# Performance work log

Hardware: AMD Instinct MI355X
Metric: run time of the kernel (lower is better)

The kernel has to match this reference:

```python
import jax, jax.numpy as jnp
import numpy as np

V, D, H, L, FF, C = 32000, 512, 8, 3, 2048, 6
B, S = 32, 1024


def setup_inputs() -> dict:
    key = jax.random.key(0)
    ks = jax.random.split(key, 8)
    tokens = jax.random.randint(ks[0], (B, S), 0, V, dtype=jnp.int32)
    emb = jax.random.normal(ks[1], (V, D), dtype=jnp.float32) * 0.02
    qkv_w = jax.random.normal(ks[2], (L, D, 3 * D), dtype=jnp.float32) * (D ** -0.5)
    qkv_b = jnp.zeros((L, 3 * D), dtype=jnp.float32)
    fc_w = jax.random.normal(ks[3], (L, D, D), dtype=jnp.float32) * (D ** -0.5)
    fc_b = jnp.zeros((L, D), dtype=jnp.float32)
    gamma = jnp.ones((D,), dtype=jnp.float32)
    beta = jnp.zeros((D,), dtype=jnp.float32)
    fc1_w = jax.random.normal(ks[4], (D, FF), dtype=jnp.float32) * (D ** -0.5)
    fc1_b = jnp.zeros((FF,), dtype=jnp.float32)
    fc2_w = jax.random.normal(ks[5], (FF, C), dtype=jnp.float32) * (FF ** -0.5)
    fc2_b = jnp.zeros((C,), dtype=jnp.float32)
    return dict(tokens=tokens, emb=emb, qkv_w=qkv_w, qkv_b=qkv_b, fc_w=fc_w,
                fc_b=fc_b, gamma=gamma, beta=beta, fc1_w=fc1_w, fc1_b=fc1_b,
                fc2_w=fc2_w, fc2_b=fc2_b)


def _sinusoidal_pe(seq_len, dim):
    pos = jnp.arange(seq_len, dtype=jnp.float32)[:, None]
    div = jnp.exp(jnp.arange(0, dim, 2).astype(jnp.float32) * (-np.log(10000.0) / dim))
    pe = jnp.zeros((seq_len, dim), dtype=jnp.float32)
    pe = pe.at[:, 0::2].set(jnp.sin(pos * div))
    pe = pe.at[:, 1::2].set(jnp.cos(pos * div))
    return pe


def reference(tokens, emb, qkv_w, qkv_b, fc_w, fc_b, gamma, beta, fc1_w, fc1_b, fc2_w, fc2_b):
    b, s = tokens.shape
    dh = D // H
    scale = dh ** -0.5

    def layernorm(y):
        m = y.mean(-1, keepdims=True)
        v = ((y - m) ** 2).mean(-1, keepdims=True)
        return (y - m) * jax.lax.rsqrt(v + 1e-5) * gamma + beta

    x = emb[tokens] + _sinusoidal_pe(s, D)[None]  # [B,S,D]
    for l in range(L):
        qkv = (x @ qkv_w[l] + qkv_b[l]).reshape(b, s, H, 3, dh)
        q = qkv[..., 0, :].transpose(0, 2, 1, 3)  # [B,H,S,dh]
        k = qkv[..., 1, :].transpose(0, 2, 1, 3)
        v = qkv[..., 2, :].transpose(0, 2, 1, 3)
        attn = jax.nn.softmax(jnp.einsum('bhqd,bhkd->bhqk', q, k) * scale, axis=-1)
        o = jnp.einsum('bhqk,bhkd->bhqd', attn, v).transpose(0, 2, 1, 3).reshape(b, s, D)
        o = o @ fc_w[l] + fc_b[l]
        x = layernorm(o + x)
    pooled = x.mean(axis=1)  # [B,D]
    h = jax.nn.relu(pooled @ fc1_w + fc1_b)  # dropout is identity at inference
    return h @ fc2_w + fc2_b
```

## Files before the change

kernel.cpp:

```cpp
#include <hip/hip_runtime.h>
#include <cmath>

#define BS_TOK 32768
#define DMODEL 512
#define NHEAD 8
#define DHEAD 64
#define NLAYER 3
#define FFDIM 2048
#define NCLS 6
#define BATCH 32
#define SEQ 1024
#define QKVW 1536

typedef short short8 __attribute__((ext_vector_type(8)));
typedef float float4v __attribute__((ext_vector_type(4)));
#define MFMA_BF16 __builtin_amdgcn_mfma_f32_16x16x32_bf16
#define QSCALE 0.18033688011112042f

__device__ __forceinline__ unsigned short f2bf(float x) {
    return (unsigned short)((__float_as_uint(x) + 0x8000u) >> 16);
}

__global__ __launch_bounds__(128) void embed_pe_kernel(const int* __restrict__ tokens,
                                                       const float* __restrict__ emb,
                                                       float* __restrict__ X,
                                                       unsigned short* __restrict__ Xb) {
    int t = blockIdx.x;
    int pos = t & (SEQ - 1);
    int tok = tokens[t];
    int d0 = threadIdx.x * 4;
    float4 e = *(const float4*)(emb + (size_t)tok * DMODEL + d0);
    const float c = -9.210340371976184f / 512.0f;
    float div0 = expf((float)d0 * c);
    float div1 = expf((float)(d0 + 2) * c);
    float a0 = (float)pos * div0;
    float a1 = (float)pos * div1;
    e.x += sinf(a0); e.y += cosf(a0);
    e.z += sinf(a1); e.w += cosf(a1);
    *(float4*)(X + (size_t)t * DMODEL + d0) = e;
    *(ushort4*)(Xb + (size_t)t * DMODEL + d0) =
        make_ushort4(f2bf(e.x), f2bf(e.y), f2bf(e.z), f2bf(e.w));
}

__global__ __launch_bounds__(256) void transcvt_kernel(const float* __restrict__ in,
                                                       unsigned short* __restrict__ out,
                                                       int R, int C) {
    __shared__ float t[32][33];
    size_t base = (size_t)blockIdx.z * R * C;
    int c0 = blockIdx.x * 32, r0 = blockIdx.y * 32;
    int tx = threadIdx.x & 31, ty = threadIdx.x >> 5;
#pragma unroll
    for (int i = 0; i < 4; i++)
        t[ty + i * 8][tx] = in[base + (size_t)(r0 + ty + i * 8) * C + c0 + tx];
    __syncthreads();
#pragma unroll
    for (int i = 0; i < 4; i++)
        out[base + (size_t)(c0 + ty + i * 8) * R + r0 + tx] = f2bf(t[tx][ty + i * 8]);
}

__global__ __launch_bounds__(256) void transcvt_qkv_kernel(const float* __restrict__ in,
                                                           unsigned short* __restrict__ out) {
    __shared__ float t[32][33];
    int l = blockIdx.z;
    int n0 = blockIdx.x * 32, r0 = blockIdx.y * 32;
    int seg = n0 >> 9, nn = n0 & 511, h = nn >> 6, d0 = nn & 63;
    int c0 = h * 192 + seg * 64 + d0;
    float s = (seg == 0) ? QSCALE : 1.f;
    const float* inp = in + (size_t)l * DMODEL * QKVW;
    unsigned short* op = out + (size_t)l * QKVW * DMODEL;
    int tx = threadIdx.x & 31, ty = threadIdx.x >> 5;
#pragma unroll
    for (int i = 0; i < 4; i++)
        t[ty + i * 8][tx] = inp[(size_t)(r0 + ty + i * 8) * QKVW + c0 + tx];
    __syncthreads();
#pragma unroll
    for (int i = 0; i < 4; i++)
        op[(size_t)(n0 + ty + i * 8) * DMODEL + r0 + tx] = f2bf(t[tx][ty + i * 8] * s);
}

__global__ __launch_bounds__(256) void permbias_kernel(const float* __restrict__ qkv_b,
                                                       float* __restrict__ pb) {
    int i = blockIdx.x * 256 + threadIdx.x;
    int l = i / QKVW, n = i - l * QKVW;
    int seg = n >> 9, nn = n & 511, h = nn >> 6, d = nn & 63;
    float s = (seg == 0) ? QSCALE : 1.f;
    pb[i] = qkv_b[l * QKVW + h * 192 + seg * 64 + d] * s;
}

__global__ __launch_bounds__(256) void gemm_qkv_kernel(const unsigned short* __restrict__ A,
                                                       const unsigned short* __restrict__ Bt,
                                                       const float* __restrict__ pb,
                                                       unsigned short* __restrict__ QKc,
                                                       unsigned short* __restrict__ Vt,
                                                       int M) {
    __shared__ unsigned short As[128 * 40];
    __shared__ unsigned short Bs[128 * 40];
    int bm = blockIdx.y * 128, bn = blockIdx.x * 128;
    int tid = threadIdx.x;
    int w = tid >> 6, lane = tid & 63, l15 = lane & 15, quad = lane >> 4;
    int wm = (w & 1) * 64, wn = (w >> 1) * 64;

    float4v acc[4][4];
    float4v z = {0.f, 0.f, 0.f, 0.f};
#pragma unroll
    for (int i = 0; i < 4; i++)
#pragma unroll
        for (int j = 0; j < 4; j++) acc[i][j] = z;

    int r0 = tid >> 2, o0 = (tid & 3) * 8;
    int r1 = (tid + 256) >> 2, o1 = (tid & 3) * 8;

    for (int k0 = 0; k0 < DMODEL; k0 += 32) {
        __syncthreads();
        *(short8*)&As[r0 * 40 + o0] = *(const short8*)(A + (size_t)(bm + r0) * DMODEL + k0 + o0);
        *(short8*)&As[r1 * 40 + o1] = *(const short8*)(A + (size_t)(bm + r1) * DMODEL + k0 + o1);
        *(short8*)&Bs[r0 * 40 + o0] = *(const short8*)(Bt + (size_t)(bn + r0) * DMODEL + k0 + o0);
        *(short8*)&Bs[r1 * 40 + o1] = *(const short8*)(Bt + (size_t)(bn + r1) * DMODEL + k0 + o1);
        __syncthreads();
        short8 af[4], bf[4];
#pragma unroll
        for (int i = 0; i < 4; i++)
            af[i] = *(short8*)&As[(wm + i * 16 + l15) * 40 + quad * 8];
#pragma unroll
        for (int j = 0; j < 4; j++)
            bf[j] = *(short8*)&Bs[(wn + j * 16 + l15) * 40 + quad * 8];
#pragma unroll
        for (int i = 0; i < 4; i++)
#pragma unroll
            for (int j = 0; j < 4; j++)
                acc[i][j] = MFMA_BF16(af[i], bf[j], acc[i][j], 0, 0, 0);
    }

    float bj[4];
#pragma unroll
    for (int j = 0; j < 4; j++) bj[j] = pb[bn + wn + j * 16 + l15];

    if (bn < 1024) {
#pragma unroll
        for (int i = 0; i < 4; i++)
#pragma unroll
            for (int r = 0; r < 4; r++) {
                size_t row = (size_t)(bm + wm + i * 16 + quad * 4 + r);
#pragma unroll
                for (int j = 0; j < 4; j++)
                    QKc[row * 1024 + bn + wn + j * 16 + l15] = f2bf(acc[i][j][r] + bj[j]);
            }
    } else {
        int bl = bm >> 10;
        int sbase = (bm & 1023) + wm;
#pragma unroll
        for (int j = 0; j < 4; j++) {
            int colp = bn - 1024 + wn + j * 16 + l15;
            int h = colp >> 6, d = colp & 63;
            unsigned short* vb = Vt + ((size_t)(bl * 8 + h) * 64 + d) * 1024 + sbase;
#pragma unroll
            for (int i = 0; i < 4; i++) {
                ushort4 v4 = make_ushort4(f2bf(acc[i][j][0] + bj[j]),
                                          f2bf(acc[i][j][1] + bj[j]),
                                          f2bf(acc[i][j][2] + bj[j]),
                                          f2bf(acc[i][j][3] + bj[j]));
                *(ushort4*)(vb + i * 16 + quad * 4) = v4;
            }
        }
    }
}

__global__ __launch_bounds__(256) void attn_kernel(const unsigned short* __restrict__ QKc,
                                                   const unsigned short* __restrict__ Vt,
                                                   unsigned short* __restrict__ O) {
    __shared__ unsigned short Ks[64 * 72];
    __shared__ unsigned short Vts[64 * 72];
    __shared__ unsigned short Ps[4 * 32 * 72];
    int bh = blockIdx.y;
    int b = bh >> 3, h = bh & 7;
    int q0 = blockIdx.x * 128;
    int tid = threadIdx.x;
    int w = tid >> 6, lane = tid & 63, l15 = lane & 15, quad = lane >> 4;
    unsigned short* Psb = &Ps[w * 32 * 72];
    const unsigned short* Kg = QKc + (size_t)b * SEQ * 1024 + 512 + h * 64;
    const unsigned short* Vg = Vt + (size_t)bh * 64 * 1024;

    short8 qf[2][2];
#pragma unroll
    for (int i = 0; i < 2; i++) {
        const unsigned short* qb =
            QKc + (size_t)(b * SEQ + q0 + w * 32 + i * 16 + l15) * 1024 + h * 64;
        qf[i][0] = *(const short8*)(qb + quad * 8);
        qf[i][1] = *(const short8*)(qb + 32 + quad * 8);
    }

    float lsum[2][4] = {{0.f, 0.f, 0.f, 0.f}, {0.f, 0.f, 0.f, 0.f}};
    float4v accO[2][4];
    float4v z = {0.f, 0.f, 0.f, 0.f};
#pragma unroll
    for (int i = 0; i < 2; i++)
#pragma unroll
        for (int dc = 0; dc < 4; dc++) accO[i][dc] = z;

    int sr = tid >> 2, so = (tid & 3) * 16;

    for (int jt = 0; jt < SEQ / 64; jt++) {
        __syncthreads();
        {
            const unsigned short* kg = Kg + (size_t)(jt * 64 + sr) * 1024 + so;
            *(short8*)&Ks[sr * 72 + so] = *(const short8*)kg;
            *(short8*)&Ks[sr * 72 + so + 8] = *(const short8*)(kg + 8);
            const unsigned short* vg = Vg + (size_t)sr * 1024 + jt * 64 + so;
            *(short8*)&Vts[sr * 72 + so] = *(const short8*)vg;
            *(short8*)&Vts[sr * 72 + so + 8] = *(const short8*)(vg + 8);
        }
        __syncthreads();

        float4v sv[2][4];
#pragma unroll
        for (int jc = 0; jc < 4; jc++) {
            short8 kf0 = *(short8*)&Ks[(jc * 16 + l15) * 72 + quad * 8];
            short8 kf1 = *(short8*)&Ks[(jc * 16 + l15) * 72 + 32 + quad * 8];
#pragma unroll
            for (int i = 0; i < 2; i++) {
                float4v s = MFMA_BF16(qf[i][0], kf0, z, 0, 0, 0);
                sv[i][jc] = MFMA_BF16(qf[i][1], kf1, s, 0, 0, 0);
            }
        }

#pragma unroll
        for (int i = 0; i < 2; i++)
#pragma unroll
            for (int jc = 0; jc < 4; jc++)
#pragma unroll
                for (int r = 0; r < 4; r++) {
                    float p = exp2f(sv[i][jc][r]);
                    lsum[i][r] += p;
                    Psb[(i * 16 + quad * 4 + r) * 72 + jc * 16 + l15] = f2bf(p);
                }

        short8 pf[2][2];
#pragma unroll
        for (int i = 0; i < 2; i++) {
            pf[i][0] = *(short8*)&Psb[(i * 16 + l15) * 72 + quad * 8];
            pf[i][1] = *(short8*)&Psb[(i * 16 + l15) * 72 + 32 + quad * 8];
        }

#pragma unroll
        for (int dc = 0; dc < 4; dc++) {
            short8 vf0 = *(short8*)&Vts[(dc * 16 + l15) * 72 + quad * 8];
            short8 vf1 = *(short8*)&Vts[(dc * 16 + l15) * 72 + 32 + quad * 8];
#pragma unroll
            for (int i = 0; i < 2; i++) {
                accO[i][dc] = MFMA_BF16(pf[i][0], vf0, accO[i][dc], 0, 0, 0);
                accO[i][dc] = MFMA_BF16(pf[i][1], vf1, accO[i][dc], 0, 0, 0);
            }
        }
    }

#pragma unroll
    for (int i = 0; i < 2; i++)
#pragma unroll
        for (int r = 0; r < 4; r++) {
            float s = lsum[i][r];
#pragma unroll
            for (int mask = 1; mask < 16; mask <<= 1) s += __shfl_xor(s, mask);
            float rinv = 1.f / s;
            size_t row = (size_t)(b * SEQ + q0 + w * 32 + i * 16 + quad * 4 + r);
#pragma unroll
            for (int dc = 0; dc < 4; dc++)
                O[row * DMODEL + h * DHEAD + dc * 16 + l15] = f2bf(accO[i][dc][r] * rinv);
        }
}

__global__ __launch_bounds__(256) void proj_ln_kernel(const unsigned short* __restrict__ A,
                                                      const unsigned short* __restrict__ Bt,
                                                      const float* __restrict__ bias,
                                                      const float* __restrict__ gamma,
                                                      const float* __restrict__ beta,
                                                      float* __restrict__ X,
                                                      unsigned short* __restrict__ Xb) {
    __shared__ unsigned short As[32 * 40];
    __shared__ unsigned short Bs[512 * 40];
    __shared__ float redS[4][32], redQ[4][32];
    int bm = blockIdx.x * 32;
    int tid = threadIdx.x;
    int w = tid >> 6, lane = tid & 63, l15 = lane & 15, quad = lane >> 4;
    int wn = w * 128;

    float4v acc[2][8];
    float4v z = {0.f, 0.f, 0.f, 0.f};
#pragma unroll
    for (int i = 0; i < 2; i++)
#pragma unroll
        for (int j = 0; j < 8; j++) acc[i][j] = z;

    for (int k0 = 0; k0 < DMODEL; k0 += 32) {
        __syncthreads();
        if (tid < 128) {
            int r = tid >> 2, o = (tid & 3) * 8;
            *(short8*)&As[r * 40 + o] = *(const short8*)(A + (size_t)(bm + r) * DMODEL + k0 + o);
        }
#pragma unroll
        for (int u = 0; u < 8; u++) {
            int c = tid + u * 256;
            int r = c >> 2, o = (c & 3) * 8;
            *(short8*)&Bs[r * 40 + o] = *(const short8*)(Bt + (size_t)r * DMODEL + k0 + o);
        }
        __syncthreads();
        short8 af[2];
#pragma unroll
        for (int i = 0; i < 2; i++)
            af[i] = *(short8*)&As[(i * 16 + l15) * 40 + quad * 8];
#pragma unroll
        for (int j = 0; j < 8; j++) {
            short8 bf = *(short8*)&Bs[(wn + j * 16 + l15) * 40 + quad * 8];
            acc[0][j] = MFMA_BF16(af[0], bf, acc[0][j], 0, 0, 0);
            acc[1][j] = MFMA_BF16(af[1], bf, acc[1][j], 0, 0, 0);
        }
    }

    float bj[8], g[8], be[8];
#pragma unroll
    for (int j = 0; j < 8; j++) {
        int col = wn + j * 16 + l15;
        bj[j] = bias[col]; g[j] = gamma[col]; be[j] = beta[col];
    }

    float o[2][4][8];
#pragma unroll
    for (int i = 0; i < 2; i++)
#pragma unroll
        for (int r = 0; r < 4; r++) {
            int lrow = i * 16 + quad * 4 + r;
            size_t row = (size_t)(bm + lrow);
            float ss = 0.f, qq = 0.f;
#pragma unroll
            for (int j = 0; j < 8; j++) {
                float v = acc[i][j][r] + bj[j] + X[row * DMODEL + wn + j * 16 + l15];
                o[i][r][j] = v; ss += v; qq += v * v;
            }
#pragma unroll
            for (int mask = 1; mask < 16; mask <<= 1) {
                ss += __shfl_xor(ss, mask);
                qq += __shfl_xor(qq, mask);
            }
            if (l15 == 0) { redS[w][lrow] = ss; redQ[w][lrow] = qq; }
        }
    __syncthreads();
#pragma unroll
    for (int i = 0; i < 2; i++)
#pragma unroll
        for (int r = 0; r < 4; r++) {
            int lrow = i * 16 + quad * 4 + r;
            float S = redS[0][lrow] + redS[1][lrow] + redS[2][lrow] + redS[3][lrow];
            float Q = redQ[0][lrow] + redQ[1][lrow] + redQ[2][lrow] + redQ[3][lrow];
            float mean = S * (1.f / 512.f);
            float var = Q * (1.f / 512.f) - mean * mean;
            float rstd = rsqrtf(var + 1e-5f);
            size_t row = (size_t)(bm + lrow);
#pragma unroll
            for (int j = 0; j < 8; j++) {
                float n = (o[i][r][j] - mean) * rstd * g[j] + be[j];
                X[row * DMODEL + wn + j * 16 + l15] = n;
                Xb[row * DMODEL + wn + j * 16 + l15] = f2bf(n);
            }
        }
}

__global__ __launch_bounds__(256) void zero_kernel(float* __restrict__ p) {
    p[blockIdx.x * 256 + threadIdx.x] = 0.f;
}
__global__ __launch_bounds__(128) void pool_kernel(const float* __restrict__ X,
                                                   float* __restrict__ pooled) {
    int b = blockIdx.x, ch = blockIdx.y;
    int d0 = threadIdx.x * 4;
    float4 acc = make_float4(0.f, 0.f, 0.f, 0.f);
    const float* base = X + (size_t)(b * SEQ + ch * 64) * DMODEL + d0;
    for (int s2 = 0; s2 < 64; s2++) {
        float4 v = *(const float4*)(base + (size_t)s2 * DMODEL);
        acc.x += v.x; acc.y += v.y; acc.z += v.z; acc.w += v.w;
    }
    atomicAdd(pooled + b * DMODEL + d0 + 0, acc.x);
    atomicAdd(pooled + b * DMODEL + d0 + 1, acc.y);
    atomicAdd(pooled + b * DMODEL + d0 + 2, acc.z);
    atomicAdd(pooled + b * DMODEL + d0 + 3, acc.w);
}

__global__ __launch_bounds__(256) void fc1_kernel(const float* __restrict__ pooled,
                                                  const float* __restrict__ fc1_w,
                                                  const float* __restrict__ fc1_b,
                                                  float* __restrict__ h) {
    __shared__ float p[DMODEL];
    int ffc = blockIdx.x, b = blockIdx.y;
    int tid = threadIdx.x;
    p[tid] = pooled[b * DMODEL + tid] * (1.f / 1024.f);
    p[tid + 256] = pooled[b * DMODEL + tid + 256] * (1.f / 1024.f);
    __syncthreads();
    int ff = ffc * 256 + tid;
    float acc = fc1_b[ff];
    for (int k = 0; k < DMODEL; k++) acc += p[k] * fc1_w[(size_t)k * FFDIM + ff];
    h[(size_t)b * FFDIM + ff] = fmaxf(acc, 0.f);
}

__global__ __launch_bounds__(256) void fc2_kernel(const float* __restrict__ h,
                                                  const float* __restrict__ fc2_w,
                                                  const float* __restrict__ fc2_b,
                                                  float* __restrict__ out) {
    __shared__ float red[NCLS][256];
    int b = blockIdx.x, tid = threadIdx.x;
    float a[NCLS];
#pragma unroll
    for (int c = 0; c < NCLS; c++) a[c] = 0.f;
    int k0 = tid * 8;
#pragma unroll
    for (int u = 0; u < 8; u++) {
        float hv = h[(size_t)b * FFDIM + k0 + u];
#pragma unroll
        for (int c = 0; c < NCLS; c++) a[c] += hv * fc2_w[(k0 + u) * NCLS + c];
    }
#pragma unroll
    for (int c = 0; c < NCLS; c++) red[c][tid] = a[c];
    __syncthreads();
    if (tid < NCLS) {
        float s = 0.f;
        for (int i = 0; i < 256; i++) s += red[tid][i];
        out[b * NCLS + tid] = s + fc2_b[tid];
    }
}

extern "C" void kernel_launch(void* const* d_in, const int* in_sizes, int n_in,
                              void* d_out, int out_size, void* d_ws, size_t ws_size,
                              hipStream_t stream) {
    const int* tokens = (const int*)d_in[0];
    const float* emb = (const float*)d_in[1];
    const float* qkv_w = (const float*)d_in[2];
    const float* qkv_b = (const float*)d_in[3];
    const float* fc_w = (const float*)d_in[4];
    const float* fc_b = (const float*)d_in[5];
    const float* gamma = (const float*)d_in[6];
    const float* beta = (const float*)d_in[7];
    const float* fc1_w = (const float*)d_in[8];
    const float* fc1_b = (const float*)d_in[9];
    const float* fc2_w = (const float*)d_in[10];
    const float* fc2_b = (const float*)d_in[11];
    float* out = (float*)d_out;

    char* p = (char*)d_ws;
    float* X = (float*)p;                         p += (size_t)BS_TOK * DMODEL * 4;
    unsigned short* Xb = (unsigned short*)p;      p += (size_t)BS_TOK * DMODEL * 2;
    float* pooled = (float*)p;                    p += (size_t)BATCH * DMODEL * 4;
    float* hbuf = (float*)p;                      p += (size_t)BATCH * FFDIM * 4;
    float* pb = (float*)p;                        p += (size_t)NLAYER * QKVW * 4;
    unsigned short* qkv_wbt = (unsigned short*)p; p += (size_t)NLAYER * QKVW * DMODEL * 2;
    unsigned short* fc_wt = (unsigned short*)p;   p += (size_t)NLAYER * DMODEL * DMODEL * 2;
    size_t fixed_bytes = (size_t)(p - (char*)d_ws);
    size_t per_batch = (size_t)SEQ * 1024 * 2 + (size_t)NHEAD * 64 * SEQ * 2
                     + (size_t)SEQ * DMODEL * 2;
    int chunkB = 1;
    for (int cb = 32; cb >= 1; cb >>= 1)
        if (fixed_bytes + (size_t)cb * per_batch <= ws_size) { chunkB = cb; break; }
    unsigned short* QKc = (unsigned short*)p;     p += (size_t)chunkB * SEQ * 1024 * 2;
    unsigned short* Vt = (unsigned short*)p;      p += (size_t)chunkB * NHEAD * 64 * SEQ * 2;
    unsigned short* Oc = (unsigned short*)p;
    int rows = chunkB * SEQ;
    int nchunks = BATCH / chunkB;

    embed_pe_kernel<<<BS_TOK, 128, 0, stream>>>(tokens, emb, X, Xb);
    permbias_kernel<<<NLAYER * QKVW / 256, 256, 0, stream>>>(qkv_b, pb);
    transcvt_qkv_kernel<<<dim3(QKVW / 32, DMODEL / 32, NLAYER), 256, 0, stream>>>(
        qkv_w, qkv_wbt);
    transcvt_kernel<<<dim3(DMODEL / 32, DMODEL / 32, NLAYER), 256, 0, stream>>>(
        fc_w, fc_wt, DMODEL, DMODEL);

    for (int l = 0; l < NLAYER; l++) {
        for (int c = 0; c < nchunks; c++) {
            unsigned short* Xbc = Xb + (size_t)c * rows * DMODEL;
            float* Xc = X + (size_t)c * rows * DMODEL;
            gemm_qkv_kernel<<<dim3(QKVW / 128, rows / 128), 256, 0, stream>>>(
                Xbc, qkv_wbt + (size_t)l * QKVW * DMODEL, pb + (size_t)l * QKVW,
                QKc, Vt, rows);
            attn_kernel<<<dim3(SEQ / 128, chunkB * NHEAD), 256, 0, stream>>>(QKc, Vt, Oc);
            proj_ln_kernel<<<rows / 32, 256, 0, stream>>>(
                Oc, fc_wt + (size_t)l * DMODEL * DMODEL, fc_b + (size_t)l * DMODEL,
                gamma, beta, Xc, Xbc);
        }
    }

    zero_kernel<<<BATCH * DMODEL / 256, 256, 0, stream>>>(pooled);
    pool_kernel<<<dim3(BATCH, 16), 128, 0, stream>>>(X, pooled);
    fc1_kernel<<<dim3(FFDIM / 256, BATCH), 256, 0, stream>>>(pooled, fc1_w, fc1_b, hbuf);
    fc2_kernel<<<BATCH, 256, 0, stream>>>(hbuf, fc2_w, fc2_b, out);
}
```

Measured before the change: 1.028 ms.

## Enlarge attention query tile and compute transposed S^T tiles for row-wise P writes

The attention kernel now gives each wave 64 query rows instead of 32, so each K/V tile staged in shared memory is reused across twice as many queries. The MFMA operands are swapped to compute S^T, which lets each lane hold one query row and write P as packed 8-byte stores and O as vector stores, and it cuts the row-sum reduction to two shuffles. The grid is reordered so heads map to blockIdx.x, and launch bounds request 2 blocks per CU. In exchange, register and shared-memory pressure per block rise, and the grid has half as many blocks.

```diff
diff --git a/kernel.cpp b/kernel.cpp
--- a/kernel.cpp
+++ b/kernel.cpp
@@ -165,107 +165,98 @@
     }
 }
 
-__global__ __launch_bounds__(256) void attn_kernel(const unsigned short* __restrict__ QKc,
-                                                   const unsigned short* __restrict__ Vt,
-                                                   unsigned short* __restrict__ O) {
+__global__ __launch_bounds__(256, 2) void attn_kernel(const unsigned short* __restrict__ QKc,
+                                                      const unsigned short* __restrict__ Vt,
+                                                      unsigned short* __restrict__ O) {
     __shared__ unsigned short Ks[64 * 72];
     __shared__ unsigned short Vts[64 * 72];
-    __shared__ unsigned short Ps[4 * 32 * 72];
-    int bh = blockIdx.y;
+    __shared__ unsigned short Ps[4 * 64 * 72];
+    int bh = blockIdx.x;
     int b = bh >> 3, h = bh & 7;
-    int q0 = blockIdx.x * 128;
+    int q0 = blockIdx.y * 256;
     int tid = threadIdx.x;
     int w = tid >> 6, lane = tid & 63, l15 = lane & 15, quad = lane >> 4;
-    unsigned short* Psb = &Ps[w * 32 * 72];
+    unsigned short* Psb = &Ps[w * 64 * 72];
     const unsigned short* Kg = QKc + (size_t)b * SEQ * 1024 + 512 + h * 64;
     const unsigned short* Vg = Vt + (size_t)bh * 64 * 1024;
 
-    short8 qf[2][2];
-#pragma unroll
-    for (int i = 0; i < 2; i++) {
+    short8 qf[4][2];
+#pragma unroll
+    for (int nt = 0; nt < 4; nt++) {
         const unsigned short* qb =
-            QKc + (size_t)(b * SEQ + q0 + w * 32 + i * 16 + l15) * 1024 + h * 64;
-        qf[i][0] = *(const short8*)(qb + quad * 8);
-        qf[i][1] = *(const short8*)(qb + 32 + quad * 8);
-    }
-
-    float lsum[2][4] = {{0.f, 0.f, 0.f, 0.f}, {0.f, 0.f, 0.f, 0.f}};
-    float4v accO[2][4];
+            QKc + (size_t)(b * SEQ + q0 + w * 64 + nt * 16 + l15) * 1024 + h * 64;
+        qf[nt][0] = *(const short8*)(qb + quad * 8);
+        qf[nt][1] = *(const short8*)(qb + 32 + quad * 8);
+    }
+
+    float lsum[4] = {0.f, 0.f, 0.f, 0.f};
+    float4v accO[4][4];
     float4v z = {0.f, 0.f, 0.f, 0.f};
 #pragma unroll
-    for (int i = 0; i < 2; i++)
-#pragma unroll
-        for (int dc = 0; dc < 4; dc++) accO[i][dc] = z;
-
-    int sr = tid >> 2, so = (tid & 3) * 16;
+    for (int dt = 0; dt < 4; dt++)
+#pragma unroll
+        for (int nt = 0; nt < 4; nt++) accO[dt][nt] = z;
 
     for (int jt = 0; jt < SEQ / 64; jt++) {
         __syncthreads();
-        {
-            const unsigned short* kg = Kg + (size_t)(jt * 64 + sr) * 1024 + so;
-            *(short8*)&Ks[sr * 72 + so] = *(const short8*)kg;
-            *(short8*)&Ks[sr * 72 + so + 8] = *(const short8*)(kg + 8);
-            const unsigned short* vg = Vg + (size_t)sr * 1024 + jt * 64 + so;
-            *(short8*)&Vts[sr * 72 + so] = *(const short8*)vg;
-            *(short8*)&Vts[sr * 72 + so + 8] = *(const short8*)(vg + 8);
-        }
-        __syncthreads();
-
-        float4v sv[2][4];
-#pragma unroll
-        for (int jc = 0; jc < 4; jc++) {
-            short8 kf0 = *(short8*)&Ks[(jc * 16 + l15) * 72 + quad * 8];
-            short8 kf1 = *(short8*)&Ks[(jc * 16 + l15) * 72 + 32 + quad * 8];
-#pragma unroll
-            for (int i = 0; i < 2; i++) {
-                float4v s = MFMA_BF16(qf[i][0], kf0, z, 0, 0, 0);
-                sv[i][jc] = MFMA_BF16(qf[i][1], kf1, s, 0, 0, 0);
-            }
-        }
-
-#pragma unroll
-        for (int i = 0; i < 2; i++)
-#pragma unroll
-            for (int jc = 0; jc < 4; jc++)
-#pragma unroll
-                for (int r = 0; r < 4; r++) {
-                    float p = exp2f(sv[i][jc][r]);
-                    lsum[i][r] += p;
-                    Psb[(i * 16 + quad * 4 + r) * 72 + jc * 16 + l15] = f2bf(p);
-                }
-
-        short8 pf[2][2];
-#pragma unroll
-        for (int i = 0; i < 2; i++) {
-            pf[i][0] = *(short8*)&Psb[(i * 16 + l15) * 72 + quad * 8];
-            pf[i][1] = *(short8*)&Psb[(i * 16 + l15) * 72 + 32 + quad * 8];
-        }
-
-#pragma unroll
-        for (int dc = 0; dc < 4; dc++) {
-            short8 vf0 = *(short8*)&Vts[(dc * 16 + l15) * 72 + quad * 8];
-            short8 vf1 = *(short8*)&Vts[(dc * 16 + l15) * 72 + 32 + quad * 8];
-#pragma unroll
-            for (int i = 0; i < 2; i++) {
-                accO[i][dc] = MFMA_BF16(pf[i][0], vf0, accO[i][dc], 0, 0, 0);
-                accO[i][dc] = MFMA_BF16(pf[i][1], vf1, accO[i][dc], 0, 0, 0);
-            }
-        }
-    }
-
-#pragma unroll
-    for (int i = 0; i < 2; i++)
-#pragma unroll
-        for (int r = 0; r < 4; r++) {
-            float s = lsum[i][r];
-#pragma unroll
-            for (int mask = 1; mask < 16; mask <<= 1) s += __shfl_xor(s, mask);
-            float rinv = 1.f / s;
-            size_t row = (size_t)(b * SEQ + q0 + w * 32 + i * 16 + quad * 4 + r);
-#pragma unroll
-            for (int dc = 0; dc < 4; dc++)
-                O[row * DMODEL + h * DHEAD + dc * 16 + l15] = f2bf(accO[i][dc][r] * rinv);
-        }
+#pragma unroll
+        for (int cc = 0; cc < 2; cc++) {
+            int c = tid + cc * 256;
+            int r = c >> 3, o = (c & 7) * 8;
+            *(short8*)&Ks[r * 72 + o] = *(const short8*)(Kg + (size_t)(jt * 64 + r) * 1024 + o);
+            *(short8*)&Vts[r * 72 + o] = *(const short8*)(Vg + (size_t)r * 1024 + jt * 64 + o);
+        }
+        __syncthreads();
+
+#pragma unroll
+        for (int mt = 0; mt < 4; mt++) {
+            short8 kf0 = *(short8*)&Ks[(mt * 16 + l15) * 72 + quad * 8];
+            short8 kf1 = *(short8*)&Ks[(mt * 16 + l15) * 72 + 32 + quad * 8];
+#pragma unroll
+            for (int nt = 0; nt < 4; nt++) {
+                float4v sv = MFMA_BF16(kf0, qf[nt][0], z, 0, 0, 0);
+                sv = MFMA_BF16(kf1, qf[nt][1], sv, 0, 0, 0);
+                float p0 = exp2f(sv[0]), p1 = exp2f(sv[1]);
+                float p2 = exp2f(sv[2]), p3 = exp2f(sv[3]);
+                lsum[nt] += (p0 + p1) + (p2 + p3);
+                unsigned int u0 = (unsigned int)f2bf(p0) | ((unsigned int)f2bf(p1) << 16);
+                unsigned int u1 = (unsigned int)f2bf(p2) | ((unsigned int)f2bf(p3) << 16);
+                *(uint2*)&Psb[(nt * 16 + l15) * 72 + mt * 16 + quad * 4] = make_uint2(u0, u1);
+            }
+        }
+
+#pragma unroll
+        for (int kc = 0; kc < 2; kc++) {
+            short8 vf[4];
+#pragma unroll
+            for (int dt = 0; dt < 4; dt++)
+                vf[dt] = *(short8*)&Vts[(dt * 16 + l15) * 72 + kc * 32 + quad * 8];
+#pragma unroll
+            for (int nt = 0; nt < 4; nt++) {
+                short8 pfr = *(short8*)&Psb[(nt * 16 + l15) * 72 + kc * 32 + quad * 8];
+#pragma unroll
+                for (int dt = 0; dt < 4; dt++)
+                    accO[dt][nt] = MFMA_BF16(vf[dt], pfr, accO[dt][nt], 0, 0, 0);
+            }
+        }
+    }
+
+#pragma unroll
+    for (int nt = 0; nt < 4; nt++) {
+        float s = lsum[nt];
+        s += __shfl_xor(s, 16);
+        s += __shfl_xor(s, 32);
+        float rinv = 1.f / s;
+        size_t row = (size_t)(b * SEQ + q0 + w * 64 + nt * 16 + l15);
+#pragma unroll
+        for (int dt = 0; dt < 4; dt++) {
+            ushort4 o4 = make_ushort4(f2bf(accO[dt][nt][0] * rinv),
+                                      f2bf(accO[dt][nt][1] * rinv),
+                                      f2bf(accO[dt][nt][2] * rinv),
+                                      f2bf(accO[dt][nt][3] * rinv));
+            *(ushort4*)(O + row * DMODEL + h * DHEAD + dt * 16 + quad * 4) = o4;
+        }
+    }
 }
 
 __global__ __launch_bounds__(256) void proj_ln_kernel(const unsigned short* __restrict__ A,
@@ -475,7 +466,7 @@
             gemm_qkv_kernel<<<dim3(QKVW / 128, rows / 128), 256, 0, stream>>>(
                 Xbc, qkv_wbt + (size_t)l * QKVW * DMODEL, pb + (size_t)l * QKVW,
                 QKc, Vt, rows);
-            attn_kernel<<<dim3(SEQ / 128, chunkB * NHEAD), 256, 0, stream>>>(QKc, Vt, Oc);
+            attn_kernel<<<dim3(chunkB * NHEAD, SEQ / 256), 256, 0, stream>>>(QKc, Vt, Oc);
             proj_ln_kernel<<<rows / 32, 256, 0, stream>>>(
                 Oc, fc_wt + (size_t)l * DMODEL * DMODEL, fc_b + (size_t)l * DMODEL,
                 gamma, beta, Xc, Xbc);
```

Measured after the change: 1.056 ms. 1.03x slower.
